# Kernel optimization log

Measured on AMD Instinct MI355X. Metric: run time of the kernel, lower is better.

## Reference

```python
import jax, jax.numpy as jnp
import numpy as np

MARGIN = 0.3

def _pairwise_euclid(x):
    # torch.cdist(x, x, p=2): [N, N] Euclidean distances, zero-safe sqrt
    sq_norms = jnp.sum(x * x, axis=1)                       # [N]
    sq = sq_norms[:, None] + sq_norms[None, :] - 2.0 * (x @ x.T)
    sq = jnp.maximum(sq, 0.0)
    safe = jnp.where(sq > 0.0, sq, 1.0)
    return jnp.where(sq > 0.0, jnp.sqrt(safe), 0.0)

def setup_inputs() -> dict:
    key = jax.random.key(0)
    k1, k2 = jax.random.split(key)
    features = jax.random.normal(k1, (4096, 512), dtype=jnp.float32)
    labels = jax.random.randint(k2, (4096,), 0, 256, dtype=jnp.int64)
    return {"features": features, "labels": labels}

def reference(features, labels):
    n = features.shape[0]
    dist = _pairwise_euclid(features)                       # [N, N]
    pos_mask = labels[:, None] == labels[None, :]           # includes self
    neg_inf = jnp.float32(-np.inf)
    pos_inf = jnp.float32(np.inf)
    hardest_pos = jnp.max(jnp.where(pos_mask, dist, neg_inf), axis=1)   # [N]
    hardest_neg = jnp.min(jnp.where(pos_mask, pos_inf, dist), axis=1)   # [N]
    valid = jnp.sum(pos_mask, axis=1) > 1                   # >1 positives incl. self
    per_row = jax.nn.relu(hardest_pos - hardest_neg + MARGIN)
    loss = jnp.sum(jnp.where(valid, per_row, 0.0)) / n
    return loss
```

## Files before the change

kernel.cpp:

```cpp
#include <hip/hip_runtime.h>

#define NROWS 4096
#define DIM   512
#define MARGIN 0.3f

typedef _Float16 f16;
typedef _Float16 f16x8 __attribute__((ext_vector_type(8)));
typedef float    f32x4 __attribute__((ext_vector_type(4)));

__global__ void norms_init_kernel(const float* __restrict__ X,
                                  float* __restrict__ norms,
                                  unsigned* __restrict__ hp, unsigned* __restrict__ hn) {
    int wave = threadIdx.x >> 6;
    int lane = threadIdx.x & 63;
    int row  = blockIdx.x * 4 + wave;
    const float4* xr = (const float4*)(X + (size_t)row * DIM);
    float4 a = xr[lane];
    float4 b = xr[lane + 64];
    float s = a.x*a.x + a.y*a.y + a.z*a.z + a.w*a.w
            + b.x*b.x + b.y*b.y + b.z*b.z + b.w*b.w;
    #pragma unroll
    for (int o = 32; o; o >>= 1) s += __shfl_xor(s, o);
    if (lane == 0) norms[row] = s;
    int g = blockIdx.x * 256 + threadIdx.x;
    if (g < NROWS) { hp[g] = 0u; hn[g] = 0x7f800000u; }
}

__global__ void convert_kernel(const float* __restrict__ X, f16* __restrict__ Xh) {
    int g = blockIdx.x * 256 + threadIdx.x;
    int tile = g >> 9, u = g & 511;
    int R = tile >> 4, K0 = tile & 15;
    int rg = u >> 6, c = (u >> 4) & 3, r = u & 15;
    int row = R * 128 + rg * 16 + r;
    int k0  = K0 * 32 + c * 8;
    const float4* p = (const float4*)(X + (size_t)row * DIM + k0);
    float4 a = p[0], b = p[1];
    f16x8 h;
    h[0] = (f16)a.x; h[1] = (f16)a.y; h[2] = (f16)a.z; h[3] = (f16)a.w;
    h[4] = (f16)b.x; h[5] = (f16)b.y; h[6] = (f16)b.z; h[7] = (f16)b.w;
    *(f16x8*)(Xh + (size_t)g * 8) = h;
}

__device__ inline void gload_lds16(const f16* g, f16* l) {
    __builtin_amdgcn_global_load_lds(
        (const __attribute__((address_space(1))) void*)g,
        (__attribute__((address_space(3))) void*)l, 16, 0, 0);
}

__device__ inline void stage_tile(const f16* __restrict__ At, const f16* __restrict__ Bt,
                                  f16* buf, int qb, int lane) {
    const f16* base = (qb < 512) ? (At + (size_t)qb * 8) : (Bt + (size_t)(qb - 512) * 8);
    #pragma unroll
    for (int c2 = 0; c2 < 4; ++c2)
        gload_lds16(base + (size_t)(c2 * 64 + lane) * 8, buf + (size_t)(qb + c2 * 64) * 8);
}

__global__ __launch_bounds__(256, 3) void mfma_dist_kernel(
        const f16* __restrict__ Xh, const int* __restrict__ labels,
        const float* __restrict__ norms,
        unsigned* __restrict__ hp, unsigned* __restrict__ hn) {
    __shared__ __align__(16) f16 S0[8192];
    __shared__ __align__(16) f16 S1[8192];

    const int t    = threadIdx.x;
    const int lane = t & 63, w = t >> 6;
    const int l15  = lane & 15, l4 = lane >> 4;

    int bthw = blockIdx.x;
    int bt = (bthw & 7) * 66 + (bthw >> 3);

    int bx = (int)((sqrtf(8.0f * bt + 1.0f) - 1.0f) * 0.5f);
    while ((bx + 1) * (bx + 2) / 2 <= bt) ++bx;
    while (bx * (bx + 1) / 2 > bt) --bx;
    int by = bt - bx * (bx + 1) / 2;

    const int wr = w >> 1, wc = w & 1;
    const int qb = w * 256;

    const f16* Abase = Xh + (size_t)(by * 16) * 4096;
    const f16* Bbase = Xh + (size_t)(bx * 16) * 4096;

    f32x4 zero = {0.f, 0.f, 0.f, 0.f};
    f32x4 acc[4][4];
    #pragma unroll
    for (int m = 0; m < 4; ++m)
        #pragma unroll
        for (int n = 0; n < 4; ++n) acc[m][n] = zero;

    stage_tile(Abase,        Bbase,        S0, qb, lane);
    stage_tile(Abase + 4096, Bbase + 4096, S1, qb, lane);
    __builtin_amdgcn_sched_barrier(0);

    #pragma unroll
    for (int kt = 0; kt < 16; ++kt) {
        f16* cur = (kt & 1) ? S1 : S0;
        if (kt == 15) asm volatile("s_waitcnt vmcnt(0)" ::: "memory");
        else          asm volatile("s_waitcnt vmcnt(4)" ::: "memory");
        __builtin_amdgcn_s_barrier();
        __builtin_amdgcn_sched_barrier(0);

        f16x8 af[4], bf[4];
        #pragma unroll
        for (int m = 0; m < 4; ++m)
            af[m] = *(const f16x8*)&cur[(size_t)((wr * 4 + m) * 64 + l4 * 16 + l15) * 8];
        #pragma unroll
        for (int n = 0; n < 4; ++n)
            bf[n] = *(const f16x8*)&cur[(size_t)(512 + (wc * 4 + n) * 64 + l4 * 16 + l15) * 8];
        asm volatile("s_waitcnt lgkmcnt(0)" ::: "memory");
        __builtin_amdgcn_sched_barrier(0);
        __builtin_amdgcn_s_barrier();
        __builtin_amdgcn_sched_barrier(0);

        if (kt + 2 < 16)
            stage_tile(Abase + (size_t)(kt + 2) * 4096,
                       Bbase + (size_t)(kt + 2) * 4096, cur, qb, lane);
        __builtin_amdgcn_sched_barrier(0);

        #pragma unroll
        for (int m = 0; m < 4; ++m)
            #pragma unroll
            for (int n = 0; n < 4; ++n)
                acc[m][n] = __builtin_amdgcn_mfma_f32_16x16x32_f16(af[m], bf[n], acc[m][n], 0, 0, 0);
        __builtin_amdgcn_sched_barrier(0);
    }

    const int wrow = by * 128 + wr * 64;
    const int wcol = bx * 128 + wc * 64;
    const float FINF = __uint_as_float(0x7f800000u);

    int lj[4]; float nj[4];
    #pragma unroll
    for (int n = 0; n < 4; ++n) {
        int gc = wcol + n * 16 + l15; lj[n] = labels[gc]; nj[n] = norms[gc];
    }
    int li[16]; float ni[16];
    #pragma unroll
    for (int m = 0; m < 4; ++m)
        #pragma unroll
        for (int r = 0; r < 4; ++r) {
            int gr = wrow + m * 16 + l4 * 4 + r;
            li[m * 4 + r] = labels[gr]; ni[m * 4 + r] = norms[gr];
        }

    float cp[4], cn[4];
    #pragma unroll
    for (int n = 0; n < 4; ++n) { cp[n] = 0.f; cn[n] = FINF; }

    #pragma unroll
    for (int m = 0; m < 4; ++m) {
        #pragma unroll
        for (int r = 0; r < 4; ++r) {
            float rp = 0.f, rn = FINF;
            #pragma unroll
            for (int n = 0; n < 4; ++n) {
                float sq = fmaxf(fmaf(-2.f, acc[m][n][r], ni[m * 4 + r] + nj[n]), 0.f);
                bool same = (li[m * 4 + r] == lj[n]);
                rp = same ? fmaxf(rp, sq) : rp;
                rn = same ? rn : fminf(rn, sq);
                cp[n] = same ? fmaxf(cp[n], sq) : cp[n];
                cn[n] = same ? cn[n] : fminf(cn[n], sq);
            }
            #pragma unroll
            for (int o = 8; o; o >>= 1) {
                rp = fmaxf(rp, __shfl_xor(rp, o));
                rn = fminf(rn, __shfl_xor(rn, o));
            }
            if (l15 == 0) {
                int gr = wrow + m * 16 + l4 * 4 + r;
                atomicMax(&hp[gr], __float_as_uint(rp));
                atomicMin(&hn[gr], __float_as_uint(rn));
            }
        }
    }
    #pragma unroll
    for (int n = 0; n < 4; ++n) {
        float p = cp[n], q = cn[n];
        p = fmaxf(p, __shfl_xor(p, 16)); q = fminf(q, __shfl_xor(q, 16));
        p = fmaxf(p, __shfl_xor(p, 32)); q = fminf(q, __shfl_xor(q, 32));
        if (l4 == 0) {
            int gc = wcol + n * 16 + l15;
            atomicMax(&hp[gc], __float_as_uint(p));
            atomicMin(&hn[gc], __float_as_uint(q));
        }
    }
}

#define BK  32
#define PAD 68
__global__ __launch_bounds__(256) void dist_fp32_kernel(
        const float* __restrict__ X, const int* __restrict__ labels,
        const float* __restrict__ norms,
        unsigned* __restrict__ hp, unsigned* __restrict__ hn) {
    __shared__ __align__(16) float As[BK][PAD];
    __shared__ __align__(16) float Bs[BK][PAD];
    const int t  = threadIdx.x;
    const int tx = t & 15, ty = t >> 4;
    const int row0 = blockIdx.y * 64, col0 = blockIdx.x * 64;

    float acc[4][4] = {};
    for (int k0 = 0; k0 < DIM; k0 += BK) {
        #pragma unroll
        for (int l = 0; l < 2; ++l) {
            int idx = t + l * 256;
            int r = idx >> 3, fc = idx & 7;
            float4 va = *(const float4*)(X + (size_t)(row0 + r) * DIM + k0 + fc * 4);
            float4 vb = *(const float4*)(X + (size_t)(col0 + r) * DIM + k0 + fc * 4);
            As[fc*4+0][r] = va.x; As[fc*4+1][r] = va.y;
            As[fc*4+2][r] = va.z; As[fc*4+3][r] = va.w;
            Bs[fc*4+0][r] = vb.x; Bs[fc*4+1][r] = vb.y;
            Bs[fc*4+2][r] = vb.z; Bs[fc*4+3][r] = vb.w;
        }
        __syncthreads();
        #pragma unroll
        for (int kk = 0; kk < BK; ++kk) {
            float4 a = *(const float4*)&As[kk][ty * 4];
            float4 b = *(const float4*)&Bs[kk][tx * 4];
            float av[4] = {a.x, a.y, a.z, a.w};
            float bv[4] = {b.x, b.y, b.z, b.w};
            #pragma unroll
            for (int m = 0; m < 4; ++m)
                #pragma unroll
                for (int n = 0; n < 4; ++n)
                    acc[m][n] = fmaf(av[m], bv[n], acc[m][n]);
        }
        __syncthreads();
    }
    int li[4], lj[4]; float ni[4], nj[4];
    #pragma unroll
    for (int m = 0; m < 4; ++m) {
        int gi = row0 + ty * 4 + m; li[m] = labels[gi]; ni[m] = norms[gi];
    }
    #pragma unroll
    for (int n = 0; n < 4; ++n) {
        int gj = col0 + tx * 4 + n; lj[n] = labels[gj]; nj[n] = norms[gj];
    }
    #pragma unroll
    for (int m = 0; m < 4; ++m) {
        float pmax = 0.0f;
        float nmin = __uint_as_float(0x7f800000u);
        #pragma unroll
        for (int n = 0; n < 4; ++n) {
            float sq = fmaxf(ni[m] + nj[n] - 2.0f * acc[m][n], 0.0f);
            if (li[m] == lj[n]) pmax = fmaxf(pmax, sq);
            else                nmin = fminf(nmin, sq);
        }
        #pragma unroll
        for (int o = 8; o; o >>= 1) {
            pmax = fmaxf(pmax, __shfl_xor(pmax, o));
            nmin = fminf(nmin, __shfl_xor(nmin, o));
        }
        if (tx == 0) {
            int gi = row0 + ty * 4 + m;
            atomicMax(&hp[gi], __float_as_uint(pmax));
            atomicMin(&hn[gi], __float_as_uint(nmin));
        }
    }
}

__global__ __launch_bounds__(1024) void finalize_kernel(
        const unsigned* __restrict__ hp, const unsigned* __restrict__ hn,
        const int* __restrict__ labels, float* __restrict__ out) {
    __shared__ int hist[256];
    __shared__ float wsum[16];
    int t = threadIdx.x;
    if (t < 256) hist[t] = 0;
    __syncthreads();
    int4 lab = ((const int4*)labels)[t];
    atomicAdd(&hist[lab.x], 1); atomicAdd(&hist[lab.y], 1);
    atomicAdd(&hist[lab.z], 1); atomicAdd(&hist[lab.w], 1);
    __syncthreads();
    uint4 hp4 = ((const uint4*)hp)[t];
    uint4 hn4 = ((const uint4*)hn)[t];
    int      lv[4]  = {lab.x, lab.y, lab.z, lab.w};
    unsigned hpv[4] = {hp4.x, hp4.y, hp4.z, hp4.w};
    unsigned hnv[4] = {hn4.x, hn4.y, hn4.z, hn4.w};
    float v = 0.f;
    #pragma unroll
    for (int j = 0; j < 4; ++j) {
        float hpd = sqrtf(__uint_as_float(hpv[j]));
        float hnd = sqrtf(__uint_as_float(hnv[j]));
        if (hist[lv[j]] > 1) v += fmaxf(hpd - hnd + MARGIN, 0.f);
    }
    #pragma unroll
    for (int o = 32; o; o >>= 1) v += __shfl_xor(v, o);
    int lane = t & 63, wv = t >> 6;
    if (lane == 0) wsum[wv] = v;
    __syncthreads();
    if (t == 0) {
        float s = 0.f;
        #pragma unroll
        for (int i = 0; i < 16; ++i) s += wsum[i];
        out[0] = s / (float)NROWS;
    }
}

extern "C" void kernel_launch(void* const* d_in, const int* in_sizes, int n_in,
                              void* d_out, int out_size, void* d_ws, size_t ws_size,
                              hipStream_t stream) {
    const float* X      = (const float*)d_in[0];
    const int*   labels = (const int*)d_in[1];
    float* ws = (float*)d_ws;
    float*    norms = ws;
    unsigned* hp    = (unsigned*)(ws + 4096);
    unsigned* hn    = (unsigned*)(ws + 8192);
    f16*      Xh    = (f16*)((char*)d_ws + 65536);
    float*    out   = (float*)d_out;

    const size_t need = 65536 + (size_t)NROWS * DIM * sizeof(f16);

    hipLaunchKernelGGL(norms_init_kernel, dim3(NROWS/4), dim3(256), 0, stream, X, norms, hp, hn);
    if (ws_size >= need) {
        hipLaunchKernelGGL(convert_kernel,   dim3(1024), dim3(256), 0, stream, X, Xh);
        hipLaunchKernelGGL(mfma_dist_kernel, dim3(528),  dim3(256), 0, stream, Xh, labels, norms, hp, hn);
    } else {
        hipLaunchKernelGGL(dist_fp32_kernel, dim3(64, 64), dim3(256), 0, stream, X, labels, norms, hp, hn);
    }
    hipLaunchKernelGGL(finalize_kernel, dim3(1), dim3(1024), 0, stream, hp, hn, labels, out);
}
```

Before: 39.48 us.

## Fuse norm and fp16 conversion kernels; triple-buffer LDS in MFMA loop

Merges the norms/init kernel and the fp16 tile-layout conversion kernel into one prep kernel, so X is read once and one launch is dropped. In the MFMA distance kernel, LDS staging moves from double to triple buffering. The prefetch for tile kt+2 is now issued right after the barrier, before the current tile's fragments are read, which removes one barrier per iteration. LDS use per block rises from 32KB to 48KB, which may limit occupancy under the launch bounds of 3 blocks.

```diff
diff --git a/kernel.cpp b/kernel.cpp
--- a/kernel.cpp
+++ b/kernel.cpp
@@ -8,37 +8,30 @@
 typedef _Float16 f16x8 __attribute__((ext_vector_type(8)));
 typedef float    f32x4 __attribute__((ext_vector_type(4)));
 
-__global__ void norms_init_kernel(const float* __restrict__ X,
-                                  float* __restrict__ norms,
-                                  unsigned* __restrict__ hp, unsigned* __restrict__ hn) {
-    int wave = threadIdx.x >> 6;
-    int lane = threadIdx.x & 63;
+__global__ void prep_kernel(const float* __restrict__ X,
+                            float* __restrict__ norms, f16* __restrict__ Xh,
+                            unsigned* __restrict__ hp, unsigned* __restrict__ hn) {
+    int t = threadIdx.x;
+    int wave = t >> 6, lane = t & 63;
     int row  = blockIdx.x * 4 + wave;
-    const float4* xr = (const float4*)(X + (size_t)row * DIM);
-    float4 a = xr[lane];
-    float4 b = xr[lane + 64];
+    const float4* p = (const float4*)(X + (size_t)row * DIM + lane * 8);
+    float4 a = p[0], b = p[1];
     float s = a.x*a.x + a.y*a.y + a.z*a.z + a.w*a.w
             + b.x*b.x + b.y*b.y + b.z*b.z + b.w*b.w;
     #pragma unroll
     for (int o = 32; o; o >>= 1) s += __shfl_xor(s, o);
     if (lane == 0) norms[row] = s;
-    int g = blockIdx.x * 256 + threadIdx.x;
-    if (g < NROWS) { hp[g] = 0u; hn[g] = 0x7f800000u; }
-}
-
-__global__ void convert_kernel(const float* __restrict__ X, f16* __restrict__ Xh) {
-    int g = blockIdx.x * 256 + threadIdx.x;
-    int tile = g >> 9, u = g & 511;
-    int R = tile >> 4, K0 = tile & 15;
-    int rg = u >> 6, c = (u >> 4) & 3, r = u & 15;
-    int row = R * 128 + rg * 16 + r;
-    int k0  = K0 * 32 + c * 8;
-    const float4* p = (const float4*)(X + (size_t)row * DIM + k0);
-    float4 a = p[0], b = p[1];
+
     f16x8 h;
     h[0] = (f16)a.x; h[1] = (f16)a.y; h[2] = (f16)a.z; h[3] = (f16)a.w;
     h[4] = (f16)b.x; h[5] = (f16)b.y; h[6] = (f16)b.z; h[7] = (f16)b.w;
-    *(f16x8*)(Xh + (size_t)g * 8) = h;
+    int K0 = lane >> 2, c = lane & 3;
+    int R = row >> 7, rw = row & 127, rg = rw >> 4, r = rw & 15;
+    size_t unit = (size_t)(R * 16 + K0) * 512 + rg * 64 + c * 16 + r;
+    *(f16x8*)(Xh + unit * 8) = h;
+
+    int g = blockIdx.x * 256 + t;
+    if (g < NROWS) { hp[g] = 0u; hn[g] = 0x7f800000u; }
 }
 
 __device__ inline void gload_lds16(const f16* g, f16* l) {
@@ -59,8 +52,7 @@
         const f16* __restrict__ Xh, const int* __restrict__ labels,
         const float* __restrict__ norms,
         unsigned* __restrict__ hp, unsigned* __restrict__ hn) {
-    __shared__ __align__(16) f16 S0[8192];
-    __shared__ __align__(16) f16 S1[8192];
+    __shared__ __align__(16) f16 S[3 * 8192];
 
     const int t    = threadIdx.x;
     const int lane = t & 63, w = t >> 6;
@@ -87,35 +79,32 @@
         #pragma unroll
         for (int n = 0; n < 4; ++n) acc[m][n] = zero;
 
-    stage_tile(Abase,        Bbase,        S0, qb, lane);
-    stage_tile(Abase + 4096, Bbase + 4096, S1, qb, lane);
+    stage_tile(Abase,        Bbase,        S,        qb, lane);
+    stage_tile(Abase + 4096, Bbase + 4096, S + 8192, qb, lane);
     __builtin_amdgcn_sched_barrier(0);
 
     #pragma unroll
     for (int kt = 0; kt < 16; ++kt) {
-        f16* cur = (kt & 1) ? S1 : S0;
+        f16* cur = S + (kt % 3) * 8192;
         if (kt == 15) asm volatile("s_waitcnt vmcnt(0)" ::: "memory");
         else          asm volatile("s_waitcnt vmcnt(4)" ::: "memory");
-        __builtin_amdgcn_s_barrier();
-        __builtin_amdgcn_sched_barrier(0);
-
-        f16x8 af[4], bf[4];
-        #pragma unroll
-        for (int m = 0; m < 4; ++m)
-            af[m] = *(const f16x8*)&cur[(size_t)((wr * 4 + m) * 64 + l4 * 16 + l15) * 8];
-        #pragma unroll
-        for (int n = 0; n < 4; ++n)
-            bf[n] = *(const f16x8*)&cur[(size_t)(512 + (wc * 4 + n) * 64 + l4 * 16 + l15) * 8];
-        asm volatile("s_waitcnt lgkmcnt(0)" ::: "memory");
         __builtin_amdgcn_sched_barrier(0);
         __builtin_amdgcn_s_barrier();
         __builtin_amdgcn_sched_barrier(0);
 
         if (kt + 2 < 16)
             stage_tile(Abase + (size_t)(kt + 2) * 4096,
-                       Bbase + (size_t)(kt + 2) * 4096, cur, qb, lane);
+                       Bbase + (size_t)(kt + 2) * 4096,
+                       S + ((kt + 2) % 3) * 8192, qb, lane);
         __builtin_amdgcn_sched_barrier(0);
 
+        f16x8 af[4], bf[4];
+        #pragma unroll
+        for (int m = 0; m < 4; ++m)
+            af[m] = *(const f16x8*)&cur[(size_t)((wr * 4 + m) * 64 + l4 * 16 + l15) * 8];
+        #pragma unroll
+        for (int n = 0; n < 4; ++n)
+            bf[n] = *(const f16x8*)&cur[(size_t)(512 + (wc * 4 + n) * 64 + l4 * 16 + l15) * 8];
         #pragma unroll
         for (int m = 0; m < 4; ++m)
             #pragma unroll
@@ -185,6 +174,24 @@
     }
 }
 
+__global__ void norms_init_kernel(const float* __restrict__ X,
+                                  float* __restrict__ norms,
+                                  unsigned* __restrict__ hp, unsigned* __restrict__ hn) {
+    int wave = threadIdx.x >> 6;
+    int lane = threadIdx.x & 63;
+    int row  = blockIdx.x * 4 + wave;
+    const float4* xr = (const float4*)(X + (size_t)row * DIM);
+    float4 a = xr[lane];
+    float4 b = xr[lane + 64];
+    float s = a.x*a.x + a.y*a.y + a.z*a.z + a.w*a.w
+            + b.x*b.x + b.y*b.y + b.z*b.z + b.w*b.w;
+    #pragma unroll
+    for (int o = 32; o; o >>= 1) s += __shfl_xor(s, o);
+    if (lane == 0) norms[row] = s;
+    int g = blockIdx.x * 256 + threadIdx.x;
+    if (g < NROWS) { hp[g] = 0u; hn[g] = 0x7f800000u; }
+}
+
 #define BK  32
 #define PAD 68
 __global__ __launch_bounds__(256) void dist_fp32_kernel(
@@ -308,12 +315,14 @@
 
     const size_t need = 65536 + (size_t)NROWS * DIM * sizeof(f16);
 
-    hipLaunchKernelGGL(norms_init_kernel, dim3(NROWS/4), dim3(256), 0, stream, X, norms, hp, hn);
     if (ws_size >= need) {
-        hipLaunchKernelGGL(convert_kernel,   dim3(1024), dim3(256), 0, stream, X, Xh);
-        hipLaunchKernelGGL(mfma_dist_kernel, dim3(528),  dim3(256), 0, stream, Xh, labels, norms, hp, hn);
+        hipLaunchKernelGGL(prep_kernel,      dim3(NROWS/4), dim3(256), 0, stream,
+                           X, norms, Xh, hp, hn);
+        hipLaunchKernelGGL(mfma_dist_kernel, dim3(528),     dim3(256), 0, stream,
+                           Xh, labels, norms, hp, hn);
     } else {
-        hipLaunchKernelGGL(dist_fp32_kernel, dim3(64, 64), dim3(256), 0, stream, X, labels, norms, hp, hn);
+        hipLaunchKernelGGL(norms_init_kernel, dim3(NROWS/4), dim3(256), 0, stream, X, norms, hp, hn);
+        hipLaunchKernelGGL(dist_fp32_kernel,  dim3(64, 64),  dim3(256), 0, stream, X, labels, norms, hp, hn);
     }
     hipLaunchKernelGGL(finalize_kernel, dim3(1), dim3(1024), 0, stream, hp, hn, labels, out);
 }
```

New measurement: 33.94 us. -14.1%, faster.
